# Optimization experiments

Measured on AMD Instinct MI355X. Metric: run time of the kernel, lower is better.

The kernel has to match this reference:

```python
import jax, jax.numpy as jnp
import numpy as np

# Static config matching init_kwargs
B, T, GX, GY, C = 2, 5, 512, 512, 64   # batch, nsweeps, grid x, grid y, PFN out channels
VOXEL = np.array([0.2, 0.2, 8.0], np.float32)
PC_RANGE = np.array([-51.2, -51.2, -5.0, 51.2, 51.2, 3.0], np.float32)
EPS = 1e-3    # BatchNorm1d eps (det3d norm_cfg default)
N = 600_000   # total points
D_IN = 9      # 4 raw feats (x,y,z,r) + 3 cluster offsets + 2 center offsets


def setup_inputs() -> dict:
    key = jax.random.key(0)
    k1, k2, k3, k4, k5, k6 = jax.random.split(key, 6)
    xy = jax.random.uniform(k1, (N, 2), minval=-51.0, maxval=51.0)
    z = jax.random.uniform(k2, (N, 1), minval=-4.5, maxval=2.5)
    inten = jax.random.uniform(k3, (N, 1))
    b = jax.random.randint(k4, (N, 1), 0, B).astype(jnp.float32)
    t = jax.random.randint(k5, (N, 1), 0, T).astype(jnp.float32)
    # points format: [batch_id, x, y, z, intensity, time]
    points = jnp.concatenate([b, xy, z, inten, t], axis=1)
    W = jax.random.normal(k6, (D_IN, C), dtype=jnp.float32) * 0.05  # PFN linear (no bias)
    gamma = jnp.ones((C,), jnp.float32)   # BN weight
    beta = jnp.zeros((C,), jnp.float32)   # BN bias
    return {"points": points, "W": W, "gamma": gamma, "beta": beta}


def _forward(points, W, gamma, beta):
    vox = jnp.asarray(VOXEL)
    pcr = jnp.asarray(PC_RANGE)
    xyz = points[:, 1:4]
    coords_f = (xyz - pcr[:3]) / vox                       # (N,3) fractional voxel coords
    valid = ((coords_f[:, 0] >= 0) & (coords_f[:, 0] < GX)
             & (coords_f[:, 1] >= 0) & (coords_f[:, 1] < GY))
    cx = jnp.clip(coords_f[:, 0].astype(jnp.int32), 0, GX - 1)
    cy = jnp.clip(coords_f[:, 1].astype(jnp.int32), 0, GY - 1)
    bid = points[:, 0].astype(jnp.int32)
    tid = points[:, -1].astype(jnp.int32)
    nseg = B * T * GY * GX
    # pillar id flattened in (batch, time, y, x) order == canvas layout
    seg = ((bid * T + tid) * GY + cy) * GX + cx
    seg = jnp.where(valid, seg, nseg)                      # invalid points -> trash bin
    total = nseg + 1
    w = valid.astype(points.dtype)
    counts = jax.ops.segment_sum(w, seg, num_segments=total)                 # (total,)
    sums = jax.ops.segment_sum(xyz * w[:, None], seg, num_segments=total)    # (total,3)
    mean = sums / jnp.maximum(counts, 1.0)[:, None]        # scatter_mean of xyz per pillar
    f_cluster = xyz - mean[seg]                            # offset from pillar centroid
    center = (jnp.stack([cx, cy], 1).astype(points.dtype) * vox[:2]
              + vox[:2] * 0.5 + pcr[:2])
    f_center = xyz[:, :2] - center                         # offset from pillar center
    feats = jnp.concatenate([points[:, 1:5], f_cluster, f_center], axis=-1)  # (N,9)
    # PFNLayer: Linear(no bias) -> BatchNorm1d (train stats over valid pts) -> ReLU
    x = feats @ W                                          # (N,C)
    nvalid = jnp.maximum(w.sum(), 1.0)
    mu = (x * w[:, None]).sum(0) / nvalid
    var = (((x - mu) ** 2) * w[:, None]).sum(0) / nvalid   # biased var (train mode)
    x = jax.nn.relu(gamma * (x - mu) * jax.lax.rsqrt(var + EPS) + beta)
    # scatter_max over pillars, then dense canvas (empty pillars = 0)
    feat_max = jax.ops.segment_max(x, seg, num_segments=total)[:nseg]        # (nseg,C)
    canvas = jnp.where(counts[:nseg, None] > 0, feat_max, 0.0)
    canvas = canvas.reshape(B, T, GY, GX, C).transpose(0, 4, 1, 2, 3)        # (B,C,T,GY,GX)
    return canvas


def reference(points, W, gamma, beta):
    return _forward(points, W, gamma, beta)
```

## Files before the change

### kernel.cpp

```cpp
#include <hip/hip_runtime.h>
#include <stdint.h>
#include <float.h>


#define GXc 512
#define GYc 512
#define Bc  2
#define Tc  5
#define Cc  64
#define NSEG (Bc * Tc * GYc * GXc)
#define SBc 2048

__device__ __forceinline__ bool point_prep(const float* __restrict__ p,
    float& x, float& y, float& z, float& inten,
    int& bid, int& tid, int& cx, int& cy, int& seg)
{
    float b0 = p[0];
    x = p[1]; y = p[2]; z = p[3]; inten = p[4];
    float tf = p[5];
    float cf0 = __fmul_rn(__fadd_rn(x, 51.2f), 5.0f);
    float cf1 = __fmul_rn(__fadd_rn(y, 51.2f), 5.0f);
    bool valid = (cf0 >= 0.0f) && (cf0 < 512.0f) && (cf1 >= 0.0f) && (cf1 < 512.0f);
    int icx = (int)cf0; icx = icx < 0 ? 0 : (icx > GXc - 1 ? GXc - 1 : icx);
    int icy = (int)cf1; icy = icy < 0 ? 0 : (icy > GYc - 1 ? GYc - 1 : icy);
    cx = icx; cy = icy;
    bid = (int)b0;
    tid = (int)tf;
    seg = ((bid * Tc + tid) * GYc + cy) * GXc + cx;
    return valid;
}

extern "C" __global__ __launch_bounds__(256)
void k_count(const float* __restrict__ pts, uint32_t* __restrict__ counts,
             uint2* __restrict__ srArr, int n)
{
    int i = blockIdx.x * 256 + threadIdx.x;
    if (i >= n) return;
    float x, y, z, it; int bid, tid, cx, cy, seg;
    bool v = point_prep(pts + (size_t)i * 6, x, y, z, it, bid, tid, cx, cy, seg);
    if (!v) { srArr[i] = make_uint2(0xFFFFFFFFu, 0u); return; }
    uint32_t r = atomicAdd(&counts[seg], 1u);
    srArr[i] = make_uint2((uint32_t)seg, r);
}

extern "C" __global__ __launch_bounds__(1024)
void k_offsets(const uint32_t* __restrict__ counts, uint32_t* __restrict__ ctr,
               int* __restrict__ denseOf, uint32_t* __restrict__ offOf,
               int* __restrict__ segOfDense, uint2* __restrict__ cntoff)
{
    int tid = threadIdx.x;
    int i = blockIdx.x * 1024 + tid;
    uint32_t cnt = (i < NSEG) ? counts[i] : 0u;
    uint32_t occ = (cnt > 0u) ? 1u : 0u;
    unsigned long long v = ((unsigned long long)occ << 32) | (unsigned long long)cnt;
    unsigned long long inc = v;
    int lane = tid & 63, wid = tid >> 6;
    #pragma unroll
    for (int d = 1; d < 64; d <<= 1) {
        unsigned long long t = __shfl_up(inc, d, 64);
        if (lane >= d) inc += t;
    }
    __shared__ unsigned long long wtot[16];
    __shared__ unsigned long long wbase[16];
    __shared__ unsigned long long gbase;
    if (lane == 63) wtot[wid] = inc;
    __syncthreads();
    if (wid == 0) {
        unsigned long long w = (lane < 16) ? wtot[lane] : 0ull;
        unsigned long long s = w;
        #pragma unroll
        for (int d = 1; d < 16; d <<= 1) {
            unsigned long long t = __shfl_up(s, d, 64);
            if (lane >= d) s += t;
        }
        if (lane < 16) wbase[lane] = s - w;
        if (lane == 15)
            gbase = atomicAdd((unsigned long long*)(ctr + 2), s);
    }
    __syncthreads();
    if (i >= NSEG) return;
    unsigned long long ex = gbase + wbase[wid] + (inc - v);
    if (occ) {
        uint32_t d = (uint32_t)(ex >> 32);
        uint32_t o = (uint32_t)ex;
        denseOf[i] = (int)d;
        offOf[i] = o;
        segOfDense[d] = i;
        cntoff[d] = make_uint2(o, cnt);
    } else {
        denseOf[i] = -1;
    }
}

extern "C" __global__ __launch_bounds__(256)
void k_fill(const float* __restrict__ pts, const uint2* __restrict__ srArr,
            const uint32_t* __restrict__ offOf, float4* __restrict__ list4, int n)
{
    int i = blockIdx.x * 256 + threadIdx.x;
    if (i >= n) return;
    uint2 sr = srArr[i];
    if (sr.x == 0xFFFFFFFFu) return;
    const float* P = pts + (size_t)i * 6;
    list4[offOf[sr.x] + sr.y] = make_float4(P[1], P[2], P[3], P[4]);
}

extern "C" __global__ __launch_bounds__(256)
void k_pillar(const float4* __restrict__ list4, const uint2* __restrict__ cntoff,
              const int* __restrict__ segOfDense, const float* __restrict__ W,
              const uint32_t* __restrict__ ctr, float2* __restrict__ compact,
              double* __restrict__ px, double* __restrict__ px2)
{
    int lane = threadIdx.x & 63;
    int sub  = threadIdx.x >> 6;
    uint32_t nP = ctr[3];
    float w0 = W[0 * Cc + lane], w1 = W[1 * Cc + lane], w2 = W[2 * Cc + lane];
    float w3 = W[3 * Cc + lane], w4 = W[4 * Cc + lane], w5 = W[5 * Cc + lane];
    float w6 = W[6 * Cc + lane], w7 = W[7 * Cc + lane], w8 = W[8 * Cc + lane];
    float wx = w0 + w4 + w7, wy = w1 + w5 + w8, wz = w2 + w6;
    double ax = 0.0, ax2 = 0.0;
    for (uint32_t d = blockIdx.x * 4 + sub; d < nP; d += (uint32_t)gridDim.x * 4) {
        int seg = segOfDense[d];
        uint2 co = cntoff[d];
        uint32_t off = co.x, cnt = co.y;
        int cx = seg & (GXc - 1);
        int cy = (seg >> 9) & (GYc - 1);
        float ctr0 = __fadd_rn(__fadd_rn(__fmul_rn((float)cx, 0.2f), 0.1f), -51.2f);
        float ctr1 = __fadd_rn(__fadd_rn(__fmul_rn((float)cy, 0.2f), 0.1f), -51.2f);
        float cconst = -(ctr0 * w7 + ctr1 * w8);
        float sx = 0.f, sy = 0.f, sz = 0.f;
        float mx = -FLT_MAX, mn = FLT_MAX;
        double spb = 0.0, spb2 = 0.0;
        for (uint32_t p = 0; p < cnt; p++) {
            float4 P = list4[off + p];
            sx += P.x; sy += P.y; sz += P.z;
            float pb = fmaf(P.x, wx,
                       fmaf(P.y, wy,
                       fmaf(P.z, wz,
                       fmaf(P.w, w3, cconst))));
            mx = fmaxf(mx, pb);
            mn = fminf(mn, pb);
            spb += (double)pb;
            spb2 = fma((double)pb, (double)pb, spb2);
        }
        float fc = (float)cnt;
        float m0 = sx / fc, m1 = sy / fc, m2 = sz / fc;
        float md = fmaf(m0, w4, fmaf(m1, w5, m2 * w6));
        compact[(size_t)d * 64 + lane] = make_float2(mx - md, mn - md);
        double mdd = (double)md, cd = (double)cnt;
        ax  += spb - cd * mdd;
        ax2 += spb2 - 2.0 * mdd * spb + cd * mdd * mdd;
    }
    __shared__ double sred[256];
    sred[threadIdx.x] = ax;
    __syncthreads();
    if (sub == 0)
        px[(size_t)blockIdx.x * 64 + lane] =
            sred[lane] + sred[lane + 64] + sred[lane + 128] + sred[lane + 192];
    __syncthreads();
    sred[threadIdx.x] = ax2;
    __syncthreads();
    if (sub == 0)
        px2[(size_t)blockIdx.x * 64 + lane] =
            sred[lane] + sred[lane + 64] + sred[lane + 128] + sred[lane + 192];
}

extern "C" __global__ __launch_bounds__(256)
void k_finalize(const double* __restrict__ px, const double* __restrict__ px2,
                const uint32_t* __restrict__ ctr,
                const float* __restrict__ gamma, const float* __restrict__ beta,
                float* __restrict__ scale, float* __restrict__ shift)
{
    int c = threadIdx.x & 63;
    int g = threadIdx.x >> 6;
    double sx = 0.0, sx2 = 0.0;
    for (int b = g; b < SBc; b += 4) {
        sx  += px[(size_t)b * 64 + c];
        sx2 += px2[(size_t)b * 64 + c];
    }
    __shared__ double sr[256];
    sr[threadIdx.x] = sx;
    __syncthreads();
    double tsx = 0.0;
    if (g == 0) tsx = sr[c] + sr[c + 64] + sr[c + 128] + sr[c + 192];
    __syncthreads();
    sr[threadIdx.x] = sx2;
    __syncthreads();
    if (g == 0) {
        double tsx2 = sr[c] + sr[c + 64] + sr[c + 128] + sr[c + 192];
        uint32_t nvu = ctr[2];
        if (nvu < 1u) nvu = 1u;
        double nv = (double)nvu;
        double mu = tsx / nv;
        double var = tsx2 / nv - mu * mu;
        float r = (float)(1.0 / sqrt(var + 0.001));
        float sc = gamma[c] * r;
        scale[c] = sc;
        shift[c] = fmaf(-(float)mu, sc, beta[c]);
    }
}

extern "C" __global__ __launch_bounds__(256)
void k_expand(const float2* __restrict__ compact, const int* __restrict__ denseOf,
              const float* __restrict__ scale, const float* __restrict__ shift,
              float* __restrict__ out)
{
    __shared__ int sdense[128];
    __shared__ float tile[128 * 65];
    int tid = threadIdx.x;
    int s0 = blockIdx.x * 128;
    if (tid < 128) sdense[tid] = denseOf[s0 + tid];
    __syncthreads();
    int w = tid >> 6, lane = tid & 63;
    float sc = scale[lane], sh = shift[lane];
    for (int k = 0; k < 32; k++) {
        int p = w * 32 + k;
        int d = sdense[p];
        float v = 0.0f;
        if (d >= 0) {
            float2 mm = compact[(size_t)d * 64 + lane];
            float sel = (sc >= 0.0f) ? mm.x : mm.y;
            v = fmaxf(fmaf(sel, sc, sh), 0.0f);
        }
        tile[p * 65 + lane] = v;
    }
    __syncthreads();
    int gx0 = s0 & (GXc - 1);
    int gy  = (s0 >> 9) & (GYc - 1);
    int bt  = s0 >> 18;
    int t   = bt % Tc;
    int b   = bt / Tc;
    int p   = tid & 127;
    int ch  = tid >> 7;
    size_t rowbase = ((size_t)gy << 9) + gx0 + p;
    for (int cc = 0; cc < 64; cc += 2) {
        int c = cc + ch;
        size_t o = ((((size_t)b * Cc + c) * Tc + t) << 18) + rowbase;
        out[o] = tile[p * 65 + c];
    }
}

extern "C" void kernel_launch(void* const* d_in, const int* in_sizes, int n_in,
                              void* d_out, int out_size, void* d_ws, size_t ws_size,
                              hipStream_t stream)
{
    const float* pts   = (const float*)d_in[0];
    const float* W     = (const float*)d_in[1];
    const float* gamma = (const float*)d_in[2];
    const float* beta  = (const float*)d_in[3];
    int n = in_sizes[0] / 6;

    uint8_t* ws = (uint8_t*)d_ws;
    size_t npad = ((size_t)n * 4 + 255) & ~(size_t)255;
    const size_t OFF_CTR    = 0;
    const size_t OFF_COUNTS = 256;
    const size_t ZERO_END   = OFF_COUNTS + (size_t)NSEG * 4;
    const size_t OFF_PX     = ZERO_END;
    const size_t OFF_PX2    = OFF_PX  + (size_t)SBc * 64 * 8;
    const size_t OFF_SCALE  = OFF_PX2 + (size_t)SBc * 64 * 8;
    const size_t OFF_SHIFT  = OFF_SCALE + 256;
    const size_t OFF_DENSE  = OFF_SHIFT + 256;
    const size_t OFF_OFFOF  = OFF_DENSE + (size_t)NSEG * 4;
    const size_t OFF_SDENSE = OFF_OFFOF + (size_t)NSEG * 4;
    const size_t OFF_CNTOFF = OFF_SDENSE + (size_t)NSEG * 4;
    const size_t OFF_SR     = OFF_CNTOFF + (size_t)NSEG * 8;
    const size_t OFF_LIST   = OFF_SR + npad * 2;
    const size_t OFF_COMP   = OFF_LIST + npad * 4;

    uint32_t* ctr     = (uint32_t*)(ws + OFF_CTR);
    uint32_t* counts  = (uint32_t*)(ws + OFF_COUNTS);
    double*   px      = (double*)(ws + OFF_PX);
    double*   px2     = (double*)(ws + OFF_PX2);
    float*    scale   = (float*)(ws + OFF_SCALE);
    float*    shift   = (float*)(ws + OFF_SHIFT);
    int*      denseOf = (int*)(ws + OFF_DENSE);
    uint32_t* offOf   = (uint32_t*)(ws + OFF_OFFOF);
    int*      segOfD  = (int*)(ws + OFF_SDENSE);
    uint2*    cntoff  = (uint2*)(ws + OFF_CNTOFF);
    uint2*    srArr   = (uint2*)(ws + OFF_SR);
    float4*   list4   = (float4*)(ws + OFF_LIST);
    float2*   compact = (float2*)(ws + OFF_COMP);

    hipMemsetAsync(ws, 0, ZERO_END, stream);

    k_count   <<<(n + 255) / 256, 256, 0, stream>>>(pts, counts, srArr, n);
    k_offsets <<<(NSEG + 1023) / 1024, 1024, 0, stream>>>(counts, ctr, denseOf,
                                                          offOf, segOfD, cntoff);
    k_fill    <<<(n + 255) / 256, 256, 0, stream>>>(pts, srArr, offOf, list4, n);
    k_pillar  <<<SBc, 256, 0, stream>>>(list4, cntoff, segOfD, W, ctr,
                                        compact, px, px2);
    k_finalize<<<1, 256, 0, stream>>>(px, px2, ctr, gamma, beta, scale, shift);
    k_expand  <<<NSEG / 128, 256, 0, stream>>>(compact, denseOf, scale, shift,
                                               (float*)d_out);
}
```

Before: 1.154 ms.

## Use gamma sign to store one extremum, pack pillar descriptor, vectorize canvas writes

k_pillar now reads gamma's sign per channel and keeps only the relevant extremum (max of sign*pb), so the compact buffer holds one float per channel instead of a float2. This halves compact traffic in k_pillar and k_expand. The pillar descriptor (offset, count, seg) is packed into one uint4 so each pillar needs a single load. k_expand writes the canvas as float4 stores over 4 consecutive x positions instead of scalar stores, at the cost of strided LDS reads with possible bank conflicts.

```diff
diff --git a/kernel.cpp b/kernel.cpp
--- a/kernel.cpp
+++ b/kernel.cpp
@@ -46,7 +46,7 @@
 extern "C" __global__ __launch_bounds__(1024)
 void k_offsets(const uint32_t* __restrict__ counts, uint32_t* __restrict__ ctr,
                int* __restrict__ denseOf, uint32_t* __restrict__ offOf,
-               int* __restrict__ segOfDense, uint2* __restrict__ cntoff)
+               uint4* __restrict__ qdesc)
 {
     int tid = threadIdx.x;
     int i = blockIdx.x * 1024 + tid;
@@ -85,8 +85,7 @@
         uint32_t o = (uint32_t)ex;
         denseOf[i] = (int)d;
         offOf[i] = o;
-        segOfDense[d] = i;
-        cntoff[d] = make_uint2(o, cnt);
+        qdesc[d] = make_uint4(o, cnt, (uint32_t)i, 0u);
     } else {
         denseOf[i] = -1;
     }
@@ -105,9 +104,9 @@
 }
 
 extern "C" __global__ __launch_bounds__(256)
-void k_pillar(const float4* __restrict__ list4, const uint2* __restrict__ cntoff,
-              const int* __restrict__ segOfDense, const float* __restrict__ W,
-              const uint32_t* __restrict__ ctr, float2* __restrict__ compact,
+void k_pillar(const float4* __restrict__ list4, const uint4* __restrict__ qdesc,
+              const float* __restrict__ W, const float* __restrict__ gamma,
+              const uint32_t* __restrict__ ctr, float* __restrict__ compact,
               double* __restrict__ px, double* __restrict__ px2)
 {
     int lane = threadIdx.x & 63;
@@ -117,18 +116,19 @@
     float w3 = W[3 * Cc + lane], w4 = W[4 * Cc + lane], w5 = W[5 * Cc + lane];
     float w6 = W[6 * Cc + lane], w7 = W[7 * Cc + lane], w8 = W[8 * Cc + lane];
     float wx = w0 + w4 + w7, wy = w1 + w5 + w8, wz = w2 + w6;
+    float sgn = (gamma[lane] >= 0.0f) ? 1.0f : -1.0f;
     double ax = 0.0, ax2 = 0.0;
     for (uint32_t d = blockIdx.x * 4 + sub; d < nP; d += (uint32_t)gridDim.x * 4) {
-        int seg = segOfDense[d];
-        uint2 co = cntoff[d];
-        uint32_t off = co.x, cnt = co.y;
+        uint4 q = qdesc[d];
+        uint32_t off = q.x, cnt = q.y;
+        int seg = (int)q.z;
         int cx = seg & (GXc - 1);
         int cy = (seg >> 9) & (GYc - 1);
         float ctr0 = __fadd_rn(__fadd_rn(__fmul_rn((float)cx, 0.2f), 0.1f), -51.2f);
         float ctr1 = __fadd_rn(__fadd_rn(__fmul_rn((float)cy, 0.2f), 0.1f), -51.2f);
         float cconst = -(ctr0 * w7 + ctr1 * w8);
         float sx = 0.f, sy = 0.f, sz = 0.f;
-        float mx = -FLT_MAX, mn = FLT_MAX;
+        float m = -FLT_MAX;
         double spb = 0.0, spb2 = 0.0;
         for (uint32_t p = 0; p < cnt; p++) {
             float4 P = list4[off + p];
@@ -137,15 +137,14 @@
                        fmaf(P.y, wy,
                        fmaf(P.z, wz,
                        fmaf(P.w, w3, cconst))));
-            mx = fmaxf(mx, pb);
-            mn = fminf(mn, pb);
+            m = fmaxf(m, sgn * pb);
             spb += (double)pb;
             spb2 = fma((double)pb, (double)pb, spb2);
         }
         float fc = (float)cnt;
         float m0 = sx / fc, m1 = sy / fc, m2 = sz / fc;
         float md = fmaf(m0, w4, fmaf(m1, w5, m2 * w6));
-        compact[(size_t)d * 64 + lane] = make_float2(mx - md, mn - md);
+        compact[(size_t)d * 64 + lane] = sgn * m - md;
         double mdd = (double)md, cd = (double)cnt;
         ax  += spb - cd * mdd;
         ax2 += spb2 - 2.0 * mdd * spb + cd * mdd * mdd;
@@ -200,7 +199,7 @@
 }
 
 extern "C" __global__ __launch_bounds__(256)
-void k_expand(const float2* __restrict__ compact, const int* __restrict__ denseOf,
+void k_expand(const float* __restrict__ compact, const int* __restrict__ denseOf,
               const float* __restrict__ scale, const float* __restrict__ shift,
               float* __restrict__ out)
 {
@@ -217,9 +216,8 @@
         int d = sdense[p];
         float v = 0.0f;
         if (d >= 0) {
-            float2 mm = compact[(size_t)d * 64 + lane];
-            float sel = (sc >= 0.0f) ? mm.x : mm.y;
-            v = fmaxf(fmaf(sel, sc, sh), 0.0f);
+            float val = compact[(size_t)d * 64 + lane];
+            v = fmaxf(fmaf(val, sc, sh), 0.0f);
         }
         tile[p * 65 + lane] = v;
     }
@@ -229,13 +227,19 @@
     int bt  = s0 >> 18;
     int t   = bt % Tc;
     int b   = bt / Tc;
-    int p   = tid & 127;
-    int ch  = tid >> 7;
-    size_t rowbase = ((size_t)gy << 9) + gx0 + p;
-    for (int cc = 0; cc < 64; cc += 2) {
-        int c = cc + ch;
+    int q   = tid & 31;
+    int cq  = tid >> 5;
+    size_t rowbase = ((size_t)gy << 9) + gx0 + q * 4;
+    #pragma unroll
+    for (int cc = 0; cc < 64; cc += 8) {
+        int c = cc + cq;
+        float4 vv;
+        vv.x = tile[(q * 4 + 0) * 65 + c];
+        vv.y = tile[(q * 4 + 1) * 65 + c];
+        vv.z = tile[(q * 4 + 2) * 65 + c];
+        vv.w = tile[(q * 4 + 3) * 65 + c];
         size_t o = ((((size_t)b * Cc + c) * Tc + t) << 18) + rowbase;
-        out[o] = tile[p * 65 + c];
+        *reinterpret_cast<float4*>(out + o) = vv;
     }
 }
 
@@ -260,9 +264,8 @@
     const size_t OFF_SHIFT  = OFF_SCALE + 256;
     const size_t OFF_DENSE  = OFF_SHIFT + 256;
     const size_t OFF_OFFOF  = OFF_DENSE + (size_t)NSEG * 4;
-    const size_t OFF_SDENSE = OFF_OFFOF + (size_t)NSEG * 4;
-    const size_t OFF_CNTOFF = OFF_SDENSE + (size_t)NSEG * 4;
-    const size_t OFF_SR     = OFF_CNTOFF + (size_t)NSEG * 8;
+    const size_t OFF_QDESC  = OFF_OFFOF + (size_t)NSEG * 4;
+    const size_t OFF_SR     = OFF_QDESC + (size_t)NSEG * 16;
     const size_t OFF_LIST   = OFF_SR + npad * 2;
     const size_t OFF_COMP   = OFF_LIST + npad * 4;
 
@@ -274,19 +277,18 @@
     float*    shift   = (float*)(ws + OFF_SHIFT);
     int*      denseOf = (int*)(ws + OFF_DENSE);
     uint32_t* offOf   = (uint32_t*)(ws + OFF_OFFOF);
-    int*      segOfD  = (int*)(ws + OFF_SDENSE);
-    uint2*    cntoff  = (uint2*)(ws + OFF_CNTOFF);
+    uint4*    qdesc   = (uint4*)(ws + OFF_QDESC);
     uint2*    srArr   = (uint2*)(ws + OFF_SR);
     float4*   list4   = (float4*)(ws + OFF_LIST);
-    float2*   compact = (float2*)(ws + OFF_COMP);
+    float*    compact = (float*)(ws + OFF_COMP);
 
     hipMemsetAsync(ws, 0, ZERO_END, stream);
 
     k_count   <<<(n + 255) / 256, 256, 0, stream>>>(pts, counts, srArr, n);
     k_offsets <<<(NSEG + 1023) / 1024, 1024, 0, stream>>>(counts, ctr, denseOf,
-                                                          offOf, segOfD, cntoff);
+                                                          offOf, qdesc);
     k_fill    <<<(n + 255) / 256, 256, 0, stream>>>(pts, srArr, offOf, list4, n);
-    k_pillar  <<<SBc, 256, 0, stream>>>(list4, cntoff, segOfD, W, ctr,
+    k_pillar  <<<SBc, 256, 0, stream>>>(list4, qdesc, W, gamma, ctr,
                                         compact, px, px2);
     k_finalize<<<1, 256, 0, stream>>>(px, px2, ctr, gamma, beta, scale, shift);
     k_expand  <<<NSEG / 128, 256, 0, stream>>>(compact, denseOf, scale, shift,
```

New measurement: 1.129 ms. 2.2% less time.
